# Kernel optimization log

Hardware: AMD Instinct MI355X
Metric: run time of the kernel (lower is better)

## Reference

```python
import jax, jax.numpy as jnp
import numpy as np

N, F_IN, HID, OUT, K, L = 16000, 16, 256, 128, 8, 3


def setup_inputs() -> dict:
    key = jax.random.key(0)
    ks = jax.random.split(key, 8)
    rn = lambda k, sh, sc: (jax.random.normal(k, sh, jnp.float32) * sc)
    return {
        "x": rn(ks[0], (N, F_IN), 1.0),
        "coords": rn(ks[1], (N, 3), 1.0),
        "We": rn(ks[2], (F_IN, HID), 0.1),
        "be": jnp.zeros((HID,), jnp.float32),
        "gnn_W": rn(ks[3], (L, HID, HID), 0.05),
        "gnn_b": jnp.zeros((L, HID), jnp.float32),
        "Wp1": rn(ks[4], (HID, HID // 2), 0.05),
        "bp1": jnp.zeros((HID // 2,), jnp.float32),
        "Wp2": rn(ks[5], (HID // 2, OUT), 0.05),
        "bp2": jnp.zeros((OUT,), jnp.float32),
    }


def knn_edges(coords, k=K):
    # squared pairwise distances (same ordering as torch.cdist) -> kNN, drop self
    sq = jnp.sum(coords * coords, axis=1)
    d2 = sq[:, None] + sq[None, :] - 2.0 * (coords @ coords.T)  # [N, N]
    _, idx = jax.lax.top_k(-d2, k + 1)            # smallest k+1 (incl. self)
    nbr = idx[:, 1:]                               # [N, k]
    src = jnp.broadcast_to(jnp.arange(coords.shape[0])[:, None], nbr.shape)
    return src.reshape(-1), nbr.reshape(-1)       # edge_index rows


def gcn_layer(h, W, b, src, dst, n):
    # GCN with added self-loops and symmetric degree normalization
    deg = jnp.ones((n,), h.dtype).at[dst].add(1.0)   # in-degree + self-loop
    norm = jax.lax.rsqrt(deg)
    hw = h @ W                                        # [N, HID]
    msg = hw[src] * (norm[src] * norm[dst])[:, None]  # gather + scale
    agg = jax.ops.segment_sum(msg, dst, num_segments=n)
    agg = agg + hw * (norm * norm)[:, None]           # self-loop term
    return agg + b


def reference(x, coords, We, be, gnn_W, gnn_b, Wp1, bp1, Wp2, bp2):
    n = x.shape[0]
    src, dst = knn_edges(coords)
    h = x @ We + be                     # survey encoder -> [N, HID]
    for i in range(L):
        h = gcn_layer(h, gnn_W[i], gnn_b[i], src, dst, n)
        h = jax.nn.relu(h)              # dropout is identity in eval mode
    g = jnp.mean(h, axis=0)             # mean pooling (batch=None) -> [HID]
    out = jax.nn.relu(g @ Wp1 + bp1) @ Wp2 + bp2  # output projection -> [OUT]
    return out
```

## Files before the change

### kernel.cpp

```cpp
#include <hip/hip_runtime.h>
#include <math.h>

#define N_NODES 16000
#define F_IN    16
#define HID     256
#define OUTD    128
#define KNN     8
#define LAYERS  3
#define NEDGE   (N_NODES * KNN)

#define NPAD    16384
#define PARTS   4
#define PART_SZ (NPAD / PARTS)
#define SEGS    32
#define NMIN    (PARTS * SEGS)
#define CAPP    32

typedef __attribute__((ext_vector_type(8))) short  s8v;
typedef __attribute__((ext_vector_type(4))) float  f4v;

__device__ __forceinline__ unsigned short f2bf(float x) {
    unsigned u = __float_as_uint(x);
    unsigned r = u + 0x7fffu + ((u >> 16) & 1u);
    return (unsigned short)(r >> 16);
}
__device__ __forceinline__ float bf2f(unsigned short b) {
    return __uint_as_float(((unsigned)b) << 16);
}

__global__ __launch_bounds__(256) void prep_kernel(const float* __restrict__ coords,
                                                   float4* __restrict__ cand,
                                                   int4* __restrict__ zeroA,
                                                   int4* __restrict__ zeroB) {
    int i = blockIdx.x * 256 + threadIdx.x;
    int4 z4 = {0, 0, 0, 0};
    if (i < 8000) zeroA[i] = z4;
    if (i < 4096) zeroB[i] = z4;
    if (i >= NPAD) return;
    if (i < N_NODES) {
        float x = coords[3 * i], y = coords[3 * i + 1], z2 = coords[3 * i + 2];
        cand[i] = make_float4(-2.f * x, -2.f * y, -2.f * z2, x * x + y * y + z2 * z2);
    } else {
        cand[i] = make_float4(0.f, 0.f, 0.f, INFINITY);
    }
}

#define DIST(qx, qy, qz, c) fmaf(qx, c.x, fmaf(qy, c.y, fmaf(qz, c.z, c.w)))

__global__ __launch_bounds__(256) void knn_min_kernel(const float* __restrict__ coords,
                                                      const float4* __restrict__ cand,
                                                      float* __restrict__ minv) {
    int tid  = threadIdx.x;
    int seg  = tid & 31;
    int qg   = tid >> 5;
    int qbase = blockIdx.x * 64;
    int part = blockIdx.y;

    float qx[8], qy[8], qz[8], m[8];
#pragma unroll
    for (int i = 0; i < 8; ++i) {
        int q = qbase + i * 8 + qg;
        qx[i] = coords[q * 3]; qy[i] = coords[q * 3 + 1]; qz[i] = coords[q * 3 + 2];
        m[i] = INFINITY;
    }

    int pbase = part * PART_SZ;
#pragma unroll 2
    for (int c0 = 0; c0 < PART_SZ; c0 += 128) {
        float4 v0 = cand[pbase + c0 + seg];
        float4 v1 = cand[pbase + c0 + seg + 32];
        float4 v2 = cand[pbase + c0 + seg + 64];
        float4 v3 = cand[pbase + c0 + seg + 96];
#pragma unroll
        for (int i = 0; i < 8; ++i) {
            float d0 = DIST(qx[i], qy[i], qz[i], v0);
            float d1 = DIST(qx[i], qy[i], qz[i], v1);
            float d2 = DIST(qx[i], qy[i], qz[i], v2);
            float d3 = DIST(qx[i], qy[i], qz[i], v3);
            m[i] = fminf(m[i], fminf(fminf(d0, d1), fminf(d2, d3)));
        }
    }
#pragma unroll
    for (int i = 0; i < 8; ++i) {
        int q = qbase + i * 8 + qg;
        minv[(q * PARTS + part) * SEGS + seg] = m[i];
    }
}

__global__ __launch_bounds__(256) void tau_kernel(const float* __restrict__ minv,
                                                  float* __restrict__ tau) {
    int q = blockIdx.x * 256 + threadIdx.x;
    if (q >= N_NODES) return;
    float b[9];
#pragma unroll
    for (int p = 0; p < 9; ++p) b[p] = INFINITY;
    const float4* mv = (const float4*)(minv + (size_t)q * NMIN);
#pragma unroll
    for (int c = 0; c < 16; ++c) {
        float4 a0 = mv[c * 2], a1 = mv[c * 2 + 1];
        float v = fminf(fminf(fminf(a0.x, a0.y), fminf(a0.z, a0.w)),
                        fminf(fminf(a1.x, a1.y), fminf(a1.z, a1.w)));
#pragma unroll
        for (int p = 8; p >= 1; --p) {
            bool  up = v < b[p - 1];
            b[p] = up ? b[p - 1] : (v < b[p] ? v : b[p]);
        }
        if (v < b[0]) b[0] = v;
    }
    tau[q] = b[8];
}

__global__ __launch_bounds__(256) void knn_collect_kernel(const float* __restrict__ coords,
                                                          const float4* __restrict__ cand,
                                                          const float* __restrict__ tau,
                                                          int* __restrict__ cnt,
                                                          float2* __restrict__ cl) {
    __shared__ int scnt[64];
    int tid  = threadIdx.x;
    int seg  = tid & 31;
    int qg   = tid >> 5;
    int qbase = blockIdx.x * 64;
    int part  = blockIdx.y;

    float qx[8], qy[8], qz[8], tt[8];
#pragma unroll
    for (int i = 0; i < 8; ++i) {
        int q = qbase + i * 8 + qg;
        qx[i] = coords[q * 3]; qy[i] = coords[q * 3 + 1]; qz[i] = coords[q * 3 + 2];
        tt[i] = tau[q];
    }
    if (tid < 64) scnt[tid] = 0;
    __syncthreads();

    int pbase = part * PART_SZ;
#pragma unroll 2
    for (int c0 = 0; c0 < PART_SZ; c0 += 128) {
        float4 v0 = cand[pbase + c0 + seg];
        float4 v1 = cand[pbase + c0 + seg + 32];
        float4 v2 = cand[pbase + c0 + seg + 64];
        float4 v3 = cand[pbase + c0 + seg + 96];
        int jb = pbase + c0 + seg;
#pragma unroll
        for (int i = 0; i < 8; ++i) {
            float d0 = DIST(qx[i], qy[i], qz[i], v0);
            float d1 = DIST(qx[i], qy[i], qz[i], v1);
            float d2 = DIST(qx[i], qy[i], qz[i], v2);
            float d3 = DIST(qx[i], qy[i], qz[i], v3);
            float m4 = fminf(fminf(d0, d1), fminf(d2, d3));
            if (m4 <= tt[i]) {
                int qi = qbase + i * 8 + qg;
                int cb = (int)(((size_t)qi * PARTS + part) * CAPP);
                if (d0 <= tt[i]) {
                    int pos = atomicAdd(&scnt[i * 8 + qg], 1);
                    if (pos < CAPP) cl[cb + pos] = make_float2(d0, __int_as_float(jb));
                }
                if (d1 <= tt[i]) {
                    int pos = atomicAdd(&scnt[i * 8 + qg], 1);
                    if (pos < CAPP) cl[cb + pos] = make_float2(d1, __int_as_float(jb + 32));
                }
                if (d2 <= tt[i]) {
                    int pos = atomicAdd(&scnt[i * 8 + qg], 1);
                    if (pos < CAPP) cl[cb + pos] = make_float2(d2, __int_as_float(jb + 64));
                }
                if (d3 <= tt[i]) {
                    int pos = atomicAdd(&scnt[i * 8 + qg], 1);
                    if (pos < CAPP) cl[cb + pos] = make_float2(d3, __int_as_float(jb + 96));
                }
            }
        }
    }
    __syncthreads();
    if (tid < 64) cnt[(size_t)(qbase + tid) * PARTS + part] = scnt[tid];
}

#define INS9L(bd, bi, d, j)                                                   \
    {                                                                         \
        _Pragma("unroll")                                                     \
        for (int p = 8; p >= 1; --p) {                                        \
            bool up = (d) < bd[p-1] || ((d) == bd[p-1] && (j) < bi[p-1]);     \
            bool in = (d) < bd[p]   || ((d) == bd[p]   && (j) < bi[p]);       \
            float nd = up ? bd[p-1] : (in ? (d) : bd[p]);                     \
            int   ni = up ? bi[p-1] : (in ? (j) : bi[p]);                     \
            bd[p] = nd; bi[p] = ni;                                           \
        }                                                                     \
        if ((d) < bd[0] || ((d) == bd[0] && (j) < bi[0])) {                   \
            bd[0] = (d); bi[0] = (j);                                         \
        }                                                                     \
    }

__global__ __launch_bounds__(128) void knn_select_kernel(const float* __restrict__ coords,
                                                         const float4* __restrict__ cand,
                                                         const float2* __restrict__ cl,
                                                         const int* __restrict__ cnt,
                                                         int* __restrict__ nbr,
                                                         int* __restrict__ indeg) {
    int q = blockIdx.x * 128 + threadIdx.x;
    if (q >= N_NODES) return;
    float bd[9]; int bi[9];
#pragma unroll
    for (int p = 0; p < 9; ++p) { bd[p] = INFINITY; bi[p] = 0x7fffffff; }
    int n0 = cnt[(size_t)q * PARTS + 0];
    int n1 = cnt[(size_t)q * PARTS + 1];
    int n2 = cnt[(size_t)q * PARTS + 2];
    int n3 = cnt[(size_t)q * PARTS + 3];
    if (n0 <= CAPP && n1 <= CAPP && n2 <= CAPP && n3 <= CAPP) {
#pragma unroll
        for (int p = 0; p < PARTS; ++p) {
            int n = (p == 0) ? n0 : (p == 1) ? n1 : (p == 2) ? n2 : n3;
            const float2* segp = cl + ((size_t)q * PARTS + p) * CAPP;
            for (int i = 0; i < n; ++i) {
                float2 e = segp[i];
                float d = e.x; int j = __float_as_int(e.y);
                INS9L(bd, bi, d, j);
            }
        }
    } else {
        float qx = coords[q*3], qy = coords[q*3+1], qz = coords[q*3+2];
        for (int j = 0; j < NPAD; ++j) {
            float4 c = cand[j];
            float d = DIST(qx, qy, qz, c);
            if (d < bd[8] || (d == bd[8] && j < bi[8])) INS9L(bd, bi, d, j);
        }
    }
#pragma unroll
    for (int p = 1; p < 9; ++p) {
        nbr[q * 8 + p - 1] = bi[p];
        atomicAdd(&indeg[bi[p]], 1);
    }
}

__global__ __launch_bounds__(1024) void scan_kernel(const int* __restrict__ indeg,
                                                    int* __restrict__ offs,
                                                    float* __restrict__ norm) {
    __shared__ int ssum[1024];
    int t = threadIdx.x;
    const int CH = 16;
    int base = t * CH;
    int s = 0;
    for (int c = 0; c < CH; ++c) {
        int idx = base + c;
        if (idx < N_NODES) s += indeg[idx];
    }
    ssum[t] = s;
    __syncthreads();
    for (int d = 1; d < 1024; d <<= 1) {
        int v = (t >= d) ? ssum[t - d] : 0;
        __syncthreads();
        ssum[t] += v;
        __syncthreads();
    }
    int run = ssum[t] - s;
    for (int c = 0; c < CH; ++c) {
        int idx = base + c;
        if (idx < N_NODES) {
            int dg = indeg[idx];
            offs[idx] = run;
            run += dg;
            norm[idx] = rsqrtf((float)(1 + dg));
        }
    }
    if (t == 1023) offs[N_NODES] = ssum[1023];
}

__global__ void fill_kernel(const int* __restrict__ nbr, const int* __restrict__ offs,
                            int* __restrict__ cursor, int* __restrict__ adj) {
    int e = blockIdx.x * blockDim.x + threadIdx.x;
    if (e < NEDGE) {
        int d   = nbr[e];
        int src = e >> 3;
        int pos = atomicAdd(&cursor[d], 1);
        adj[offs[d] + pos] = src;
    }
}

__global__ __launch_bounds__(256) void gemm_kernel(const float* __restrict__ A,
                                                   const float* __restrict__ B,
                                                   unsigned short* __restrict__ C,
                                                   int K,
                                                   const float* __restrict__ bias,
                                                   const float* __restrict__ Wg,
                                                   unsigned short* __restrict__ WThi,
                                                   unsigned short* __restrict__ WTlo) {
    if (blockIdx.y == 4) {
        for (int idx = blockIdx.x * 256 + threadIdx.x; idx < LAYERS * 65536;
             idx += 64000) {
            int l = idx >> 16;
            int r = idx & 65535;
            int k = r >> 8, j = r & 255;
            float xv = Wg[idx];
            unsigned short hb = f2bf(xv);
            size_t o = (size_t)l * 65536 + j * 256 + k;
            WThi[o] = hb;
            WTlo[o] = f2bf(xv - bf2f(hb));
        }
        return;
    }
    __shared__ float As[16][68];
    __shared__ float Bs[16][64];
    int tid = threadIdx.x;
    int rowBase = blockIdx.x * 64;
    int colBase = blockIdx.y * 64;
    int rg = tid >> 4;
    int cg = tid & 15;

    int ar = tid >> 2;
    int ac = (tid & 3) * 4;
    int bk = tid >> 4;
    int bn = (tid & 15) * 4;

    float4 acc0 = {0,0,0,0}, acc1 = {0,0,0,0}, acc2 = {0,0,0,0}, acc3 = {0,0,0,0};

    for (int kb = 0; kb < K; kb += 16) {
        float4 av = *(const float4*)(A + (size_t)(rowBase + ar) * K + kb + ac);
        float4 bv = *(const float4*)(B + (size_t)(kb + bk) * HID + colBase + bn);
        __syncthreads();
        As[ac + 0][ar] = av.x; As[ac + 1][ar] = av.y;
        As[ac + 2][ar] = av.z; As[ac + 3][ar] = av.w;
        *(float4*)&Bs[bk][bn] = bv;
        __syncthreads();
#pragma unroll
        for (int k = 0; k < 16; ++k) {
            float4 a = *(const float4*)&As[k][rg * 4];
            float4 b = *(const float4*)&Bs[k][cg * 4];
            acc0.x = fmaf(a.x, b.x, acc0.x); acc0.y = fmaf(a.x, b.y, acc0.y);
            acc0.z = fmaf(a.x, b.z, acc0.z); acc0.w = fmaf(a.x, b.w, acc0.w);
            acc1.x = fmaf(a.y, b.x, acc1.x); acc1.y = fmaf(a.y, b.y, acc1.y);
            acc1.z = fmaf(a.y, b.z, acc1.z); acc1.w = fmaf(a.y, b.w, acc1.w);
            acc2.x = fmaf(a.z, b.x, acc2.x); acc2.y = fmaf(a.z, b.y, acc2.y);
            acc2.z = fmaf(a.z, b.z, acc2.z); acc2.w = fmaf(a.z, b.w, acc2.w);
            acc3.x = fmaf(a.w, b.x, acc3.x); acc3.y = fmaf(a.w, b.y, acc3.y);
            acc3.z = fmaf(a.w, b.z, acc3.z); acc3.w = fmaf(a.w, b.w, acc3.w);
        }
        __syncthreads();
    }

    int row = rowBase + rg * 4;
    int col = colBase + cg * 4;
    float4 bb = *(const float4*)(bias + col);

    ushort4 o;
    o.x = f2bf(acc0.x + bb.x); o.y = f2bf(acc0.y + bb.y);
    o.z = f2bf(acc0.z + bb.z); o.w = f2bf(acc0.w + bb.w);
    *(ushort4*)(C + (size_t)(row + 0) * HID + col) = o;
    o.x = f2bf(acc1.x + bb.x); o.y = f2bf(acc1.y + bb.y);
    o.z = f2bf(acc1.z + bb.z); o.w = f2bf(acc1.w + bb.w);
    *(ushort4*)(C + (size_t)(row + 1) * HID + col) = o;
    o.x = f2bf(acc2.x + bb.x); o.y = f2bf(acc2.y + bb.y);
    o.z = f2bf(acc2.z + bb.z); o.w = f2bf(acc2.w + bb.w);
    *(ushort4*)(C + (size_t)(row + 2) * HID + col) = o;
    o.x = f2bf(acc3.x + bb.x); o.y = f2bf(acc3.y + bb.y);
    o.z = f2bf(acc3.z + bb.z); o.w = f2bf(acc3.w + bb.w);
    *(ushort4*)(C + (size_t)(row + 3) * HID + col) = o;
}

__global__ __launch_bounds__(256) void mfma_gemm_kernel(const unsigned short* __restrict__ A,
                                                        const unsigned short* __restrict__ WThi,
                                                        const unsigned short* __restrict__ WTlo,
                                                        unsigned short* __restrict__ C,
                                                        const float* __restrict__ rowscale) {
    __shared__ unsigned short Ah[64][40];
    __shared__ unsigned short Bh[64][40], Bl[64][40];
    int tid = threadIdx.x;
    int rowBase = blockIdx.x * 64;
    int colBase = blockIdx.y * 64;
    int wave = tid >> 6;
    int lane = tid & 63;
    int fr = lane & 15;
    int fg = lane >> 4;

    int asr = tid >> 2;
    int ask = (tid & 3) * 8;

    f4v acc[4];
#pragma unroll
    for (int c = 0; c < 4; ++c) acc[c] = (f4v){0.f, 0.f, 0.f, 0.f};

    for (int kb = 0; kb < HID; kb += 32) {
        uint4 av = *(const uint4*)(A    + (size_t)(rowBase + asr) * HID + kb + ask);
        uint4 bh = *(const uint4*)(WThi + (size_t)(colBase + asr) * HID + kb + ask);
        uint4 bl = *(const uint4*)(WTlo + (size_t)(colBase + asr) * HID + kb + ask);
        __syncthreads();
        *(uint4*)&Ah[asr][ask] = av;
        *(uint4*)&Bh[asr][ask] = bh;
        *(uint4*)&Bl[asr][ask] = bl;
        __syncthreads();

        s8v af = *(s8v*)&Ah[wave * 16 + fr][fg * 8];
#pragma unroll
        for (int c = 0; c < 4; ++c) {
            s8v bfh = *(s8v*)&Bh[c * 16 + fr][fg * 8];
            s8v bfl = *(s8v*)&Bl[c * 16 + fr][fg * 8];
            acc[c] = __builtin_amdgcn_mfma_f32_16x16x32_bf16(af, bfh, acc[c], 0, 0, 0);
            acc[c] = __builtin_amdgcn_mfma_f32_16x16x32_bf16(af, bfl, acc[c], 0, 0, 0);
        }
    }

    float sc[4];
#pragma unroll
    for (int r = 0; r < 4; ++r) sc[r] = rowscale[rowBase + wave * 16 + fg * 4 + r];
#pragma unroll
    for (int c = 0; c < 4; ++c) {
        int col = colBase + c * 16 + fr;
#pragma unroll
        for (int r = 0; r < 4; ++r) {
            int row = rowBase + wave * 16 + fg * 4 + r;
            C[(size_t)row * HID + col] = f2bf(acc[c][r] * sc[r]);
        }
    }
}

__global__ __launch_bounds__(256) void agg_kernel(const unsigned short* __restrict__ u,
                                                  const float* __restrict__ norm,
                                                  const float* __restrict__ bias,
                                                  const int* __restrict__ offs,
                                                  const int* __restrict__ adj,
                                                  unsigned short* __restrict__ hout,
                                                  float* __restrict__ gsumP) {
    __shared__ float sacc[256];
    int tid  = threadIdx.x;
    int w    = tid >> 6;
    int lane = tid & 63;
    int n0 = blockIdx.x * 8 + w;
    int n1 = n0 + 4;
    const ushort4* up = (const ushort4*)u;

    ushort4 s0 = up[(size_t)n0 * 64 + lane];
    ushort4 s1 = up[(size_t)n1 * 64 + lane];
    float a0x = bf2f(s0.x), a0y = bf2f(s0.y), a0z = bf2f(s0.z), a0w = bf2f(s0.w);
    float a1x = bf2f(s1.x), a1y = bf2f(s1.y), a1z = bf2f(s1.z), a1w = bf2f(s1.w);

    int ea = offs[n0], e1a = offs[n0 + 1];
    int eb = offs[n1], e1b = offs[n1 + 1];
    while (ea < e1a || eb < e1b) {
        bool va = ea < e1a, vb = eb < e1b;
        int sa = va ? adj[ea] : 0;
        int sb = vb ? adj[eb] : 0;
        ushort4 uva = up[(size_t)sa * 64 + lane];
        ushort4 uvb = up[(size_t)sb * 64 + lane];
        if (va) { a0x += bf2f(uva.x); a0y += bf2f(uva.y);
                  a0z += bf2f(uva.z); a0w += bf2f(uva.w); }
        if (vb) { a1x += bf2f(uvb.x); a1y += bf2f(uvb.y);
                  a1z += bf2f(uvb.z); a1w += bf2f(uvb.w); }
        ea += va; eb += vb;
    }

    float nm0 = norm[n0], nm1 = norm[n1];
    float4 bb = ((const float4*)bias)[lane];
    float4 r0, r1;
    r0.x = fmaxf(fmaf(nm0, a0x, bb.x), 0.0f);
    r0.y = fmaxf(fmaf(nm0, a0y, bb.y), 0.0f);
    r0.z = fmaxf(fmaf(nm0, a0z, bb.z), 0.0f);
    r0.w = fmaxf(fmaf(nm0, a0w, bb.w), 0.0f);
    r1.x = fmaxf(fmaf(nm1, a1x, bb.x), 0.0f);
    r1.y = fmaxf(fmaf(nm1, a1y, bb.y), 0.0f);
    r1.z = fmaxf(fmaf(nm1, a1z, bb.z), 0.0f);
    r1.w = fmaxf(fmaf(nm1, a1w, bb.w), 0.0f);
    ushort4 o0, o1;
    o0.x = f2bf(r0.x); o0.y = f2bf(r0.y); o0.z = f2bf(r0.z); o0.w = f2bf(r0.w);
    o1.x = f2bf(r1.x); o1.y = f2bf(r1.y); o1.z = f2bf(r1.z); o1.w = f2bf(r1.w);
    ((ushort4*)hout)[(size_t)n0 * 64 + lane] = o0;
    ((ushort4*)hout)[(size_t)n1 * 64 + lane] = o1;

    if (gsumP) {
        sacc[tid] = 0.0f;
        __syncthreads();
        atomicAdd(&sacc[lane * 4 + 0], r0.x + r1.x);
        atomicAdd(&sacc[lane * 4 + 1], r0.y + r1.y);
        atomicAdd(&sacc[lane * 4 + 2], r0.z + r1.z);
        atomicAdd(&sacc[lane * 4 + 3], r0.w + r1.w);
        __syncthreads();
        atomicAdd(&gsumP[(blockIdx.x & 63) * 256 + tid], sacc[tid]);
    }
}

__global__ __launch_bounds__(128) void head_kernel(const float* __restrict__ gsumP,
                                                   const float* __restrict__ Wp1,
                                                   const float* __restrict__ bp1,
                                                   const float* __restrict__ Wp2,
                                                   const float* __restrict__ bp2,
                                                   float* __restrict__ out) {
    __shared__ float gl[256];
    __shared__ float hid[128];
    int t = threadIdx.x;
    const float inv = 1.0f / 16000.0f;
    float s0 = 0.f, s1 = 0.f;
    for (int p = 0; p < 64; ++p) {
        s0 += gsumP[p * 256 + t];
        s1 += gsumP[p * 256 + t + 128];
    }
    gl[t]       = s0 * inv;
    gl[t + 128] = s1 * inv;
    __syncthreads();
    float a = bp1[t];
    for (int k = 0; k < 256; ++k) a = fmaf(gl[k], Wp1[k * 128 + t], a);
    hid[t] = fmaxf(a, 0.0f);
    __syncthreads();
    float o = bp2[t];
    for (int k = 0; k < 128; ++k) o = fmaf(hid[k], Wp2[k * 128 + t], o);
    out[t] = o;
}

extern "C" void kernel_launch(void* const* d_in, const int* in_sizes, int n_in,
                              void* d_out, int out_size, void* d_ws, size_t ws_size,
                              hipStream_t stream) {
    const float* x      = (const float*)d_in[0];
    const float* coords = (const float*)d_in[1];
    const float* We     = (const float*)d_in[2];
    const float* be     = (const float*)d_in[3];
    const float* gnn_W  = (const float*)d_in[4];
    const float* gnn_b  = (const float*)d_in[5];
    const float* Wp1    = (const float*)d_in[6];
    const float* bp1    = (const float*)d_in[7];
    const float* Wp2    = (const float*)d_in[8];
    const float* bp2    = (const float*)d_in[9];
    float* out = (float*)d_out;

    char* ws = (char*)d_ws;
    unsigned short* h = (unsigned short*)(ws + 0);
    char*  ureg  = ws + 16384000;
    int*   nbr   = (int*)  (ws + 32768000);
    int*   adj   = (int*)  (ws + 33280000);
    int*   indeg = (int*)  (ws + 33792000);
    int*   cursor= (int*)  (ws + 33856000);
    int*   offs  = (int*)  (ws + 33921024);
    float* norm  = (float*)(ws + 33985152);
    float4* cand = (float4*)(ws + 34049280);

    unsigned short* u16 = (unsigned short*)ureg;
    float*  minv = (float*)ureg;
    float*  tau  = (float*)(ureg + 8192000);
    int*    cnt  = (int*)  (ureg + 8256000);
    unsigned short* WThi = (unsigned short*)(ureg + 8512000);
    unsigned short* WTlo = (unsigned short*)(ureg + 8905216);
    float*  gsumP = (float*)(ureg + 9298432);
    float2* cl   = (float2*)(ws + 0);

    prep_kernel<<<NPAD / 256, 256, 0, stream>>>(coords, cand, (int4*)indeg, (int4*)gsumP);
    knn_min_kernel<<<dim3(N_NODES / 64, PARTS), 256, 0, stream>>>(coords, cand, minv);
    tau_kernel<<<(N_NODES + 255) / 256, 256, 0, stream>>>(minv, tau);
    knn_collect_kernel<<<dim3(N_NODES / 64, PARTS), 256, 0, stream>>>(coords, cand, tau, cnt, cl);
    knn_select_kernel<<<(N_NODES + 127) / 128, 128, 0, stream>>>(coords, cand, cl, cnt, nbr, indeg);

    scan_kernel<<<1, 1024, 0, stream>>>(indeg, offs, norm);
    fill_kernel<<<(NEDGE + 255) / 256, 256, 0, stream>>>(nbr, offs, cursor, adj);

    gemm_kernel<<<dim3(N_NODES / 64, 5), 256, 0, stream>>>(x, We, h, F_IN, be,
                                                           gnn_W, WThi, WTlo);
    for (int l = 0; l < LAYERS; ++l) {
        mfma_gemm_kernel<<<dim3(N_NODES / 64, 4), 256, 0, stream>>>(
            h, WThi + (size_t)l * 65536, WTlo + (size_t)l * 65536, u16, norm);
        agg_kernel<<<N_NODES / 8, 256, 0, stream>>>(u16, norm, gnn_b + (size_t)l * HID,
                                                    offs, adj, h,
                                                    (l == LAYERS - 1) ? gsumP : nullptr);
    }
    head_kernel<<<1, 128, 0, stream>>>(gsumP, Wp1, bp1, Wp2, bp2, out);
}
```

Before: 264.6 us.

## Collect kNN candidates only from segments whose minimum passes threshold via worklist

Replaces the brute-force collect pass, which rescanned all candidates for every query, with a worklist of (query, segment) pairs whose precomputed segment minimum is within the query's tau. A wave then evaluates only the 128 candidates of each listed segment and appends hits to a per-query buffer of 64 entries using global atomics. This is meant to cut the second full N×N distance sweep down to a small fraction of segments. In exchange it adds a worklist-building kernel, heavy global atomics on a single counter, and a grid-stride loop whose length is unknown to the launch.

```diff
diff --git a/kernel.cpp b/kernel.cpp
--- a/kernel.cpp
+++ b/kernel.cpp
@@ -14,7 +14,7 @@
 #define PART_SZ (NPAD / PARTS)
 #define SEGS    32
 #define NMIN    (PARTS * SEGS)
-#define CAPP    32
+#define CAPQ    64
 
 typedef __attribute__((ext_vector_type(8))) short  s8v;
 typedef __attribute__((ext_vector_type(4))) float  f4v;
@@ -31,11 +31,13 @@
 __global__ __launch_bounds__(256) void prep_kernel(const float* __restrict__ coords,
                                                    float4* __restrict__ cand,
                                                    int4* __restrict__ zeroA,
-                                                   int4* __restrict__ zeroB) {
+                                                   int4* __restrict__ zeroB,
+                                                   int4* __restrict__ zeroC) {
     int i = blockIdx.x * 256 + threadIdx.x;
     int4 z4 = {0, 0, 0, 0};
     if (i < 8000) zeroA[i] = z4;
     if (i < 4096) zeroB[i] = z4;
+    if (i < 4001) zeroC[i] = z4;
     if (i >= NPAD) return;
     if (i < N_NODES) {
         float x = coords[3 * i], y = coords[3 * i + 1], z2 = coords[3 * i + 2];
@@ -110,67 +112,56 @@
     tau[q] = b[8];
 }
 
+__global__ __launch_bounds__(256) void wl_build_kernel(const float* __restrict__ minv,
+                                                       const float* __restrict__ tau,
+                                                       int* __restrict__ wl,
+                                                       int* __restrict__ wl_n) {
+    int e = blockIdx.x * 256 + threadIdx.x;
+    if (e >= N_NODES * 32) return;
+    int q = e >> 5;
+    float4 m = ((const float4*)minv)[e];
+    float tt = tau[q];
+    int basew = q * 128 + (e & 31) * 4;
+    if (m.x <= tt) { int p = atomicAdd(wl_n, 1); wl[p] = basew; }
+    if (m.y <= tt) { int p = atomicAdd(wl_n, 1); wl[p] = basew + 1; }
+    if (m.z <= tt) { int p = atomicAdd(wl_n, 1); wl[p] = basew + 2; }
+    if (m.w <= tt) { int p = atomicAdd(wl_n, 1); wl[p] = basew + 3; }
+}
+
 __global__ __launch_bounds__(256) void knn_collect_kernel(const float* __restrict__ coords,
                                                           const float4* __restrict__ cand,
                                                           const float* __restrict__ tau,
+                                                          const int* __restrict__ wl,
+                                                          const int* __restrict__ wl_n,
                                                           int* __restrict__ cnt,
                                                           float2* __restrict__ cl) {
-    __shared__ int scnt[64];
-    int tid  = threadIdx.x;
-    int seg  = tid & 31;
-    int qg   = tid >> 5;
-    int qbase = blockIdx.x * 64;
-    int part  = blockIdx.y;
-
-    float qx[8], qy[8], qz[8], tt[8];
-#pragma unroll
-    for (int i = 0; i < 8; ++i) {
-        int q = qbase + i * 8 + qg;
-        qx[i] = coords[q * 3]; qy[i] = coords[q * 3 + 1]; qz[i] = coords[q * 3 + 2];
-        tt[i] = tau[q];
-    }
-    if (tid < 64) scnt[tid] = 0;
-    __syncthreads();
-
-    int pbase = part * PART_SZ;
-#pragma unroll 2
-    for (int c0 = 0; c0 < PART_SZ; c0 += 128) {
-        float4 v0 = cand[pbase + c0 + seg];
-        float4 v1 = cand[pbase + c0 + seg + 32];
-        float4 v2 = cand[pbase + c0 + seg + 64];
-        float4 v3 = cand[pbase + c0 + seg + 96];
-        int jb = pbase + c0 + seg;
-#pragma unroll
-        for (int i = 0; i < 8; ++i) {
-            float d0 = DIST(qx[i], qy[i], qz[i], v0);
-            float d1 = DIST(qx[i], qy[i], qz[i], v1);
-            float d2 = DIST(qx[i], qy[i], qz[i], v2);
-            float d3 = DIST(qx[i], qy[i], qz[i], v3);
-            float m4 = fminf(fminf(d0, d1), fminf(d2, d3));
-            if (m4 <= tt[i]) {
-                int qi = qbase + i * 8 + qg;
-                int cb = (int)(((size_t)qi * PARTS + part) * CAPP);
-                if (d0 <= tt[i]) {
-                    int pos = atomicAdd(&scnt[i * 8 + qg], 1);
-                    if (pos < CAPP) cl[cb + pos] = make_float2(d0, __int_as_float(jb));
-                }
-                if (d1 <= tt[i]) {
-                    int pos = atomicAdd(&scnt[i * 8 + qg], 1);
-                    if (pos < CAPP) cl[cb + pos] = make_float2(d1, __int_as_float(jb + 32));
-                }
-                if (d2 <= tt[i]) {
-                    int pos = atomicAdd(&scnt[i * 8 + qg], 1);
-                    if (pos < CAPP) cl[cb + pos] = make_float2(d2, __int_as_float(jb + 64));
-                }
-                if (d3 <= tt[i]) {
-                    int pos = atomicAdd(&scnt[i * 8 + qg], 1);
-                    if (pos < CAPP) cl[cb + pos] = make_float2(d3, __int_as_float(jb + 96));
-                }
-            }
-        }
-    }
-    __syncthreads();
-    if (tid < 64) cnt[(size_t)(qbase + tid) * PARTS + part] = scnt[tid];
+    int gwave = (blockIdx.x * 256 + threadIdx.x) >> 6;
+    int lane  = threadIdx.x & 63;
+    int n = *wl_n;
+    int stride = gridDim.x * 4;
+    for (int it = gwave; it < n; it += stride) {
+        int w  = wl[it];
+        int q  = w >> 7;
+        int ps = w & 127;
+        int base = (ps >> 5) * PART_SZ + (ps & 31);
+        float qx = coords[3 * q], qy = coords[3 * q + 1], qz = coords[3 * q + 2];
+        float tt = tau[q];
+        int t1 = lane + 64;
+        int p0 = base + (lane >> 2) * 128 + (lane & 3) * 32;
+        int p1 = base + (t1 >> 2) * 128 + (t1 & 3) * 32;
+        float4 c0 = cand[p0];
+        float4 c1 = cand[p1];
+        float d0 = DIST(qx, qy, qz, c0);
+        float d1 = DIST(qx, qy, qz, c1);
+        if (d0 <= tt) {
+            int pos = atomicAdd(&cnt[q], 1);
+            if (pos < CAPQ) cl[(size_t)q * CAPQ + pos] = make_float2(d0, __int_as_float(p0));
+        }
+        if (d1 <= tt) {
+            int pos = atomicAdd(&cnt[q], 1);
+            if (pos < CAPQ) cl[(size_t)q * CAPQ + pos] = make_float2(d1, __int_as_float(p1));
+        }
+    }
 }
 
 #define INS9L(bd, bi, d, j)                                                   \
@@ -199,20 +190,13 @@
     float bd[9]; int bi[9];
 #pragma unroll
     for (int p = 0; p < 9; ++p) { bd[p] = INFINITY; bi[p] = 0x7fffffff; }
-    int n0 = cnt[(size_t)q * PARTS + 0];
-    int n1 = cnt[(size_t)q * PARTS + 1];
-    int n2 = cnt[(size_t)q * PARTS + 2];
-    int n3 = cnt[(size_t)q * PARTS + 3];
-    if (n0 <= CAPP && n1 <= CAPP && n2 <= CAPP && n3 <= CAPP) {
-#pragma unroll
-        for (int p = 0; p < PARTS; ++p) {
-            int n = (p == 0) ? n0 : (p == 1) ? n1 : (p == 2) ? n2 : n3;
-            const float2* segp = cl + ((size_t)q * PARTS + p) * CAPP;
-            for (int i = 0; i < n; ++i) {
-                float2 e = segp[i];
-                float d = e.x; int j = __float_as_int(e.y);
-                INS9L(bd, bi, d, j);
-            }
+    int n = cnt[q];
+    if (n <= CAPQ) {
+        const float2* segp = cl + (size_t)q * CAPQ;
+        for (int i = 0; i < n; ++i) {
+            float2 e = segp[i];
+            float d = e.x; int j = __float_as_int(e.y);
+            INS9L(bd, bi, d, j);
         }
     } else {
         float qx = coords[q*3], qy = coords[q*3+1], qz = coords[q*3+2];
@@ -526,19 +510,23 @@
     float* norm  = (float*)(ws + 33985152);
     float4* cand = (float4*)(ws + 34049280);
 
-    unsigned short* u16 = (unsigned short*)ureg;
+    float2* cl   = (float2*)(ws + 0);
+    int*    wl   = (int*)   (ws + 8192000);
     float*  minv = (float*)ureg;
     float*  tau  = (float*)(ureg + 8192000);
     int*    cnt  = (int*)  (ureg + 8256000);
+    int*    wl_n = (int*)  (ureg + 8320000);
+    unsigned short* u16 = (unsigned short*)ureg;
     unsigned short* WThi = (unsigned short*)(ureg + 8512000);
     unsigned short* WTlo = (unsigned short*)(ureg + 8905216);
     float*  gsumP = (float*)(ureg + 9298432);
-    float2* cl   = (float2*)(ws + 0);
-
-    prep_kernel<<<NPAD / 256, 256, 0, stream>>>(coords, cand, (int4*)indeg, (int4*)gsumP);
+
+    prep_kernel<<<NPAD / 256, 256, 0, stream>>>(coords, cand, (int4*)indeg,
+                                                (int4*)gsumP, (int4*)cnt);
     knn_min_kernel<<<dim3(N_NODES / 64, PARTS), 256, 0, stream>>>(coords, cand, minv);
     tau_kernel<<<(N_NODES + 255) / 256, 256, 0, stream>>>(minv, tau);
-    knn_collect_kernel<<<dim3(N_NODES / 64, PARTS), 256, 0, stream>>>(coords, cand, tau, cnt, cl);
+    wl_build_kernel<<<(N_NODES * 32 + 255) / 256, 256, 0, stream>>>(minv, tau, wl, wl_n);
+    knn_collect_kernel<<<1024, 256, 0, stream>>>(coords, cand, tau, wl, wl_n, cnt, cl);
     knn_select_kernel<<<(N_NODES + 127) / 128, 128, 0, stream>>>(coords, cand, cl, cnt, nbr, indeg);
 
     scan_kernel<<<1, 1024, 0, stream>>>(indeg, offs, norm);
```

New measurement: 695.6 us. +162.9%, slower.
